# Kernel optimization log

Measured on AMD Instinct MI355X. Metric: run time of the kernel, lower is better.

Reference implementation:

```python
import jax, jax.numpy as jnp
import numpy as np

RATIO_H = 0.2
TEMP_FACTOR = 0.1


def _composite(patch, targets, angles, temp_seeds, B, H, W):
    """Fused resize(align_corners)+temp-clamp+rotate(expand)+pad+scatter-add.
    The torch loop per target: resize patch to ps=int(h*H*0.2), add temp, clamp,
    rotate by angle with expand, zero-pad so the rotated box top-left lands at
    (y_c*H - 0.7*h_rot, x_c*W - 0.5*w_rot), then += into canvas[img_idx].
    Here this is one inverse-affine bilinear sample over the full image grid per
    target (vmapped), followed by a segment_sum over img_idx.
    """
    P = patch.shape[-1]
    p0 = patch[0]  # [P,P]; channels are identical after expand(-1,3,-1,-1)
    yy, xx = jnp.meshgrid(jnp.arange(H, dtype=jnp.float32),
                          jnp.arange(W, dtype=jnp.float32), indexing='ij')
    half = (P - 1) / 2.0

    def per_target(tgt, angle, seed):
        cx = tgt[2] * W                       # x center in pixels
        ps = tgt[5] * H * RATIO_H             # resized patch side (continuous)
        theta = angle * (np.pi / 180.0)
        c = jnp.cos(theta); s = jnp.sin(theta)
        ext = ps * (jnp.abs(c) + jnpp_abs(s)) if False else ps * (jnp.abs(c) + jnp.abs(s))  # rotated bbox side
        # top pad = y_c*H - 0.7*h_rot  ->  rotated-box center sits 0.2*h_rot above y_c
        cy = tgt[3] * H - 0.2 * ext
        dx = xx - cx; dy = yy - cy
        u = c * dx + s * dy                   # inverse rotation
        v = -s * dx + c * dy
        scale = (P - 1) / jnp.maximum(ps - 1.0, 1.0)  # align_corners resize inverse
        px = u * scale + half
        py = v * scale + half
        pt = jnp.clip(p0 + TEMP_FACTOR * seed, 0.0, 1.0)
        x0 = jnp.floor(px); y0 = jnp.floor(py)
        ix0 = x0.astype(jnp.int32); iy0 = y0.astype(jnp.int32)
        wx = px - x0; wy = py - y0
        val = jnp.zeros_like(px); cov = jnp.zeros_like(px)
        for diy, dix, w in ((0, 0, (1 - wy) * (1 - wx)), (0, 1, (1 - wy) * wx),
                            (1, 0, wy * (1 - wx)), (1, 1, wy * wx)):
            iy = iy0 + diy; ix = ix0 + dix
            ok = (iy >= 0) & (iy < P) & (ix >= 0) & (ix < P)
            vtap = pt[jnp.clip(iy, 0, P - 1), jnp.clip(ix, 0, P - 1)]
            val = val + jnp.where(ok, vtap * w, 0.0)
            cov = cov + jnp.where(ok, w, 0.0)   # mask = sampled ones
        return val, cov

    vals, covs = jax.vmap(per_target)(targets, angles, temp_seeds)  # [T,H,W]
    idx = jax.lax.stop_gradient(targets[:, 0]).astype(jnp.int32)
    patch_tf = jax.ops.segment_sum(vals, idx, num_segments=B)       # [B,H,W]
    mask_tf = jax.ops.segment_sum(covs, idx, num_segments=B)
    patch_tf = jnp.broadcast_to(patch_tf[:, None], (B, 3, H, W))
    mask_tf = jnp.broadcast_to(mask_tf[:, None], (B, 3, H, W))
    return patch_tf, mask_tf


def setup_inputs() -> dict:
    key = jax.random.key(0)
    ks = jax.random.split(key, 8)
    B, H, W, P, T = 16, 512, 512, 128, 64
    patch = jax.random.uniform(ks[0], (1, P, P), dtype=jnp.float32)
    imgs = jax.random.normal(ks[1], (B, 3, H, W), dtype=jnp.float32)
    img_idx = jax.random.randint(ks[2], (T,), 0, B).astype(jnp.float32)
    cls = jnp.zeros((T, 1), jnp.float32)
    xy = jax.random.uniform(ks[3], (T, 2), minval=0.3, maxval=0.7)
    wh = jax.random.uniform(ks[4], (T, 2), minval=0.2, maxval=0.5)
    targets = jnp.concatenate([img_idx[:, None], cls, xy, wh], axis=1)  # [T,6]
    angles = jax.random.uniform(ks[5], (T,), minval=-10.0, maxval=10.0)
    temp_seeds = jax.random.uniform(ks[6], (T,), minval=-1.0, maxval=1.0)
    return {"patch": patch, "targets": targets, "imgs": imgs,
            "angles": angles, "temp_seeds": temp_seeds}


def reference(patch, targets, imgs, angles, temp_seeds):
    B, C, H, W = imgs.shape
    return _composite(patch, targets, angles, temp_seeds, B, H, W)
```

## Files before the change

### kernel.cpp

```cpp
#include <hip/hip_runtime.h>
#include <hip/hip_bf16.h>
#include <math.h>

#define BB   16
#define HH   512
#define WW   512
#define PP   128
#define TT   64

#define TILE_W 64
#define TILE_H 4

__global__ __launch_bounds__(256)
void PatchTransformer_43490838840065_kernel(const float* __restrict__ patch,
                                            const float* __restrict__ targets,
                                            const float* __restrict__ angles,
                                            const float* __restrict__ seeds,
                                            float* __restrict__ out) {
    const int tilesX = WW / TILE_W;
    const int tilesY = HH / TILE_H;
    const int tilesPerImg = tilesX * tilesY;
    int bid = blockIdx.x;
    int img = bid / tilesPerImg;
    int tr  = bid % tilesPerImg;
    int ty  = tr / tilesX;
    int tx  = tr % tilesX;
    int x0t = tx * TILE_W;
    int y0t = ty * TILE_H;

    __shared__ float s_cx[TT], s_cy[TT], s_c[TT], s_s[TT], s_scale[TT], s_add[TT];
    __shared__ int   s_list[TT];
    __shared__ int   s_cnt;

    int tid = threadIdx.x;
    if (tid == 0) s_cnt = 0;
    __syncthreads();

    if (tid < TT) {
        int   ib = (int)targets[tid * 6 + 0];
        float cx = targets[tid * 6 + 2] * (float)WW;
        float ps = targets[tid * 6 + 5] * (float)HH * 0.2f;
        float th = angles[tid] * 0.017453292519943295f;
        float c  = cosf(th);
        float s  = sinf(th);
        float asum = fabsf(c) + fabsf(s);
        float ext  = ps * asum;
        float cy   = targets[tid * 6 + 3] * (float)HH - 0.2f * ext;
        float scale = (float)(PP - 1) / fmaxf(ps - 1.0f, 1.0f);
        s_cx[tid] = cx;  s_cy[tid] = cy;
        s_c[tid]  = c;   s_s[tid]  = s;
        s_scale[tid] = scale;
        s_add[tid]   = 0.1f * seeds[tid];

        float r = 65.0f / scale + 1.0f;
        float R = r * asum;
        bool hit = (ib == img) &&
                   (cx + R >= (float)x0t) && (cx - R <= (float)(x0t + TILE_W - 1)) &&
                   (cy + R >= (float)y0t) && (cy - R <= (float)(y0t + TILE_H - 1));
        if (hit) {
            int slot = atomicAdd(&s_cnt, 1);
            s_list[slot] = tid;
        }
    }
    __syncthreads();

    int lx = tid & (TILE_W - 1);
    int ly = tid / TILE_W;
    int x  = x0t + lx;
    int y  = y0t + ly;
    float fxp = (float)x;
    float fyp = (float)y;

    float val = 0.0f, cov = 0.0f;
    int n = s_cnt;
    for (int k = 0; k < n; ++k) {
        int t = s_list[k];
        float dx = fxp - s_cx[t];
        float dy = fyp - s_cy[t];
        float c  = s_c[t], s = s_s[t];
        float u  =  c * dx + s * dy;
        float v  = -s * dx + c * dy;
        float sc = s_scale[t];
        float px = u * sc + 63.5f;
        float py = v * sc + 63.5f;
        float fx0 = floorf(px), fy0 = floorf(py);
        int ix0 = (int)fx0, iy0 = (int)fy0;
        float wx = px - fx0, wy = py - fy0;
        float add = s_add[t];

        #pragma unroll
        for (int dyy = 0; dyy <= 1; ++dyy) {
            #pragma unroll
            for (int dxx = 0; dxx <= 1; ++dxx) {
                int iy = iy0 + dyy;
                int ix = ix0 + dxx;
                bool ok = (iy >= 0) & (iy < PP) & (ix >= 0) & (ix < PP);
                float w = (dyy ? wy : 1.0f - wy) * (dxx ? wx : 1.0f - wx);
                if (ok) {
                    float pv = patch[iy * PP + ix] + add;
                    pv = fminf(fmaxf(pv, 0.0f), 1.0f);
                    val += pv * w;
                    cov += w;
                }
            }
        }
    }

    size_t plane    = (size_t)HH * WW;
    size_t base0    = ((size_t)img * 3) * plane + (size_t)y * WW + x;
    size_t half_out = (size_t)BB * 3 * plane;
    out[base0]             = val;
    out[base0 + plane]     = val;
    out[base0 + 2 * plane] = val;
    out[half_out + base0]             = cov;
    out[half_out + base0 + plane]     = cov;
    out[half_out + base0 + 2 * plane] = cov;
}

extern "C" void kernel_launch(void* const* d_in, const int* in_sizes, int n_in,
                              void* d_out, int out_size, void* d_ws, size_t ws_size,
                              hipStream_t stream) {
    const float* patch   = (const float*)d_in[0];
    const float* targets = (const float*)d_in[1];
    const float* angles  = (const float*)d_in[3];
    const float* seeds   = (const float*)d_in[4];
    float* out = (float*)d_out;

    const int tilesPerImg = (WW / TILE_W) * (HH / TILE_H);
    dim3 grid(BB * tilesPerImg);
    dim3 block(256);
    PatchTransformer_43490838840065_kernel<<<grid, block, 0, stream>>>(
        patch, targets, angles, seeds, out);
}
```

Baseline: 136.5 us.

## Process four pixels per thread with taller tiles and vectorized float4 stores

```diff
diff --git a/kernel.cpp b/kernel.cpp
--- a/kernel.cpp
+++ b/kernel.cpp
@@ -9,7 +9,7 @@
 #define TT   64
 
 #define TILE_W 64
-#define TILE_H 4
+#define TILE_H 16
 
 __global__ __launch_bounds__(256)
 void PatchTransformer_43490838840065_kernel(const float* __restrict__ patch,
@@ -64,43 +64,49 @@
     }
     __syncthreads();
 
-    int lx = tid & (TILE_W - 1);
-    int ly = tid / TILE_W;
+    int lx = (tid & 15) * 4;
+    int ly = tid >> 4;
     int x  = x0t + lx;
     int y  = y0t + ly;
-    float fxp = (float)x;
     float fyp = (float)y;
 
-    float val = 0.0f, cov = 0.0f;
+    float val[4] = {0.f, 0.f, 0.f, 0.f};
+    float cov[4] = {0.f, 0.f, 0.f, 0.f};
+
     int n = s_cnt;
     for (int k = 0; k < n; ++k) {
         int t = s_list[k];
-        float dx = fxp - s_cx[t];
+        float c  = s_c[t], s = s_s[t];
+        float sc = s_scale[t];
+        float add = s_add[t];
         float dy = fyp - s_cy[t];
-        float c  = s_c[t], s = s_s[t];
-        float u  =  c * dx + s * dy;
-        float v  = -s * dx + c * dy;
-        float sc = s_scale[t];
-        float px = u * sc + 63.5f;
-        float py = v * sc + 63.5f;
-        float fx0 = floorf(px), fy0 = floorf(py);
-        int ix0 = (int)fx0, iy0 = (int)fy0;
-        float wx = px - fx0, wy = py - fy0;
-        float add = s_add[t];
+        float dx0 = (float)x - s_cx[t];
 
         #pragma unroll
-        for (int dyy = 0; dyy <= 1; ++dyy) {
+        for (int j = 0; j < 4; ++j) {
+            float dx = dx0 + (float)j;
+            float u  =  c * dx + s * dy;
+            float v  = -s * dx + c * dy;
+            float px = u * sc + 63.5f;
+            float py = v * sc + 63.5f;
+            float fx0 = floorf(px), fy0 = floorf(py);
+            int ix0 = (int)fx0, iy0 = (int)fy0;
+            float wx = px - fx0, wy = py - fy0;
+
             #pragma unroll
-            for (int dxx = 0; dxx <= 1; ++dxx) {
-                int iy = iy0 + dyy;
-                int ix = ix0 + dxx;
-                bool ok = (iy >= 0) & (iy < PP) & (ix >= 0) & (ix < PP);
-                float w = (dyy ? wy : 1.0f - wy) * (dxx ? wx : 1.0f - wx);
-                if (ok) {
-                    float pv = patch[iy * PP + ix] + add;
-                    pv = fminf(fmaxf(pv, 0.0f), 1.0f);
-                    val += pv * w;
-                    cov += w;
+            for (int dyy = 0; dyy <= 1; ++dyy) {
+                #pragma unroll
+                for (int dxx = 0; dxx <= 1; ++dxx) {
+                    int iy = iy0 + dyy;
+                    int ix = ix0 + dxx;
+                    bool ok = (iy >= 0) & (iy < PP) & (ix >= 0) & (ix < PP);
+                    float w = (dyy ? wy : 1.0f - wy) * (dxx ? wx : 1.0f - wx);
+                    if (ok) {
+                        float pv = patch[iy * PP + ix] + add;
+                        pv = fminf(fmaxf(pv, 0.0f), 1.0f);
+                        val[j] += pv * w;
+                        cov[j] += w;
+                    }
                 }
             }
         }
@@ -109,12 +115,14 @@
     size_t plane    = (size_t)HH * WW;
     size_t base0    = ((size_t)img * 3) * plane + (size_t)y * WW + x;
     size_t half_out = (size_t)BB * 3 * plane;
-    out[base0]             = val;
-    out[base0 + plane]     = val;
-    out[base0 + 2 * plane] = val;
-    out[half_out + base0]             = cov;
-    out[half_out + base0 + plane]     = cov;
-    out[half_out + base0 + 2 * plane] = cov;
+    float4 v4 = make_float4(val[0], val[1], val[2], val[3]);
+    float4 c4 = make_float4(cov[0], cov[1], cov[2], cov[3]);
+    *(float4*)(out + base0)                        = v4;
+    *(float4*)(out + base0 + plane)                = v4;
+    *(float4*)(out + base0 + 2 * plane)            = v4;
+    *(float4*)(out + half_out + base0)             = c4;
+    *(float4*)(out + half_out + base0 + plane)     = c4;
+    *(float4*)(out + half_out + base0 + 2 * plane) = c4;
 }
 
 extern "C" void kernel_launch(void* const* d_in, const int* in_sizes, int n_in,
```

Measured after the change: 136.4 us. Within noise of the previous version (-0.1%).
